# Optimization experiments

Measured on AMD Instinct MI355X. Metric: run time of the kernel, lower is better.

The kernel has to match this reference:

```python
import jax, jax.numpy as jnp
import numpy as np

EPS = 1e-10
BETA = 1.0  # beta passed to VectorQuantizer in Encoder_conv


def _conv(x, w, b, stride, pad):
    # x: NCHW, w: OIHW
    y = jax.lax.conv_general_dilated(x, w, window_strides=stride, padding=pad,
                                     dimension_numbers=('NCHW', 'OIHW', 'NCHW'))
    if b is not None:
        y = y + b[None, :, None, None]
    return y


def _forward(x, w_in, b_in, w_h1, b_h1, w_h2, b_h2, w_h3, b_h3,
             r0_w1, r0_w2, r1_w1, r1_w2, emb):
    relu = jax.nn.relu
    h = relu(_conv(x, w_in, b_in, (2, 2), [(1, 1), (1, 1)]))      # [B,128,256,256]
    h = relu(_conv(h, w_h1, b_h1, (4, 4), [(2, 2), (2, 2)]))      # [B,256,64,64]
    h = relu(_conv(h, w_h2, b_h2, (4, 4), [(2, 2), (2, 2)]))      # [B,256,16,16]
    h = relu(_conv(h, w_h3, b_h3, (2, 2), [(1, 1), (1, 1)]))      # [B,256,8,8]
    # ResidualBlock with 2 Residual layers: relu->conv[1,3]->relu->conv[1,1], no bias
    for wa, wb in ((r0_w1, r0_w2), (r1_w1, r1_w2)):
        t = _conv(relu(h), wa, None, (1, 1), [(0, 0), (1, 1)])
        t = _conv(relu(t), wb, None, (1, 1), [(0, 0), (0, 0)])
        h = h + t
    h = relu(h)
    # VectorQuantizer
    lat = jnp.transpose(h, (0, 2, 3, 1))                          # [B,H,W,D]
    D = emb.shape[1]
    flat = lat.reshape(-1, D)                                     # [N,D]
    dist = (jnp.sum(flat * flat, axis=1, keepdims=True)
            + jnp.sum(emb * emb, axis=1)
            - 2.0 * flat @ emb.T)                                 # [N,K]
    idx = jnp.argmin(dist, axis=1)                                # [N]
    quant = emb[idx].reshape(lat.shape)                           # [B,H,W,D]
    sg = jax.lax.stop_gradient
    e_loss = jnp.mean((sg(quant) - lat) ** 2)
    q_loss = jnp.mean((quant - sg(lat)) ** 2)
    loss = q_loss + BETA * e_loss
    quant_st = lat + sg(quant - lat)                              # straight-through
    probs = jnp.mean(jax.nn.one_hot(idx, emb.shape[0], dtype=lat.dtype), axis=0)
    perplexity = jnp.exp(-jnp.sum(probs * jnp.log(probs + EPS)))
    return jnp.transpose(quant_st, (0, 3, 1, 2)), loss, perplexity


def setup_inputs() -> dict:
    key = jax.random.key(0)
    ks = jax.random.split(key, 14)
    C_in, C, K = 3, 256, 512
    s = 0.05
    f32 = jnp.float32
    return {
        'x':     jax.random.normal(ks[0], (8, C_in, 512, 512), f32),
        'w_in':  jax.random.normal(ks[1], (C // 2, C_in, 4, 4), f32) * s,
        'b_in':  jnp.zeros((C // 2,), f32),
        'w_h1':  jax.random.normal(ks[2], (C, C // 2, 7, 7), f32) * s,
        'b_h1':  jnp.zeros((C,), f32),
        'w_h2':  jax.random.normal(ks[3], (C, C, 7, 7), f32) * s,
        'b_h2':  jnp.zeros((C,), f32),
        'w_h3':  jax.random.normal(ks[4], (C, C, 3, 3), f32) * s,
        'b_h3':  jnp.zeros((C,), f32),
        'r0_w1': jax.random.normal(ks[5], (4 * C, C, 1, 3), f32) * s,
        'r0_w2': jax.random.normal(ks[6], (C, 4 * C, 1, 1), f32) * s,
        'r1_w1': jax.random.normal(ks[7], (4 * C, C, 1, 3), f32) * s,
        'r1_w2': jax.random.normal(ks[8], (C, 4 * C, 1, 1), f32) * s,
        'emb':   jax.random.uniform(ks[9], (K, C), f32, -1.0 / K, 1.0 / K),
    }


def reference(x, w_in, b_in, w_h1, b_h1, w_h2, b_h2, w_h3, b_h3,
              r0_w1, r0_w2, r1_w1, r1_w2, emb):
    return _forward(x, w_in, b_in, w_h1, b_h1, w_h2, b_h2, w_h3, b_h3,
                    r0_w1, r0_w2, r1_w1, r1_w2, emb)
```

## Files before the change

kernel.cpp:

```cpp
#include <hip/hip_runtime.h>
#include <hip/hip_bf16.h>

typedef __hip_bfloat16 bf16;
typedef __attribute__((ext_vector_type(4))) float f32x4;
typedef __attribute__((ext_vector_type(8))) short short8;

__device__ __forceinline__ float b2f(bf16 v) { return __bfloat162float(v); }
__device__ __forceinline__ ushort f2bu(float v)
{
    bf16 b = __float2bfloat16(v);
    return *(ushort*)&b;
}
__device__ __forceinline__ uint relu2(uint v)
{
    uint r = v;
    if (r & 0x8000u)     r &= 0xFFFF0000u;
    if (r & 0x80000000u) r &= 0x0000FFFFu;
    return r;
}
__device__ __forceinline__ uint packbf2(float a, float b)
{
    uint lo = f2bu(a), hi = f2bu(b);
    return lo | (hi << 16);
}

typedef const __attribute__((address_space(1))) unsigned int* as1_u32;
typedef __attribute__((address_space(3))) unsigned int* as3_u32;
__device__ __forceinline__ void gld16(const void* g, uint* l)
{
    __builtin_amdgcn_global_load_lds((as1_u32)g, (as3_u32)l, 16, 0, 0);
}

__global__ __launch_bounds__(256) void initw_k(
        const float* __restrict__ w_in, const float* __restrict__ w_h1,
        const float* __restrict__ w_h2, const float* __restrict__ w_h3,
        const float* __restrict__ r0w1, const float* __restrict__ r0w2,
        const float* __restrict__ r1w1, const float* __restrict__ r1w2,
        const float* __restrict__ emb,
        bf16* __restrict__ wp1, bf16* __restrict__ wpack2, bf16* __restrict__ wpack3,
        bf16* __restrict__ wp4, bf16* __restrict__ wpA0, bf16* __restrict__ wpA1,
        bf16* __restrict__ wpB0, bf16* __restrict__ wpB1,
        float* __restrict__ en, float* __restrict__ mse, int* __restrict__ hist,
        float* __restrict__ zpad)
{
    __shared__ ushort ls[12544];
    int b = blockIdx.x, t = threadIdx.x;

    if (b < 256) {
        const float* src = w_h1 + (size_t)b * 6272;
        for (int i = t; i < 6272; i += 256) ls[i] = f2bu(src[i]);
        __syncthreads();
        for (int e = t; e < 800; e += 256) {
            int tap = e >> 4, cib8 = e & 15;
            short8 v;
            #pragma unroll
            for (int cil = 0; cil < 8; ++cil)
                v[cil] = (tap < 49) ? (short)ls[(cib8 * 8 + cil) * 49 + tap] : (short)0;
            *(short8*)(wpack2 + ((size_t)(tap * 16 + cib8) * 256 + b) * 8) = v;
        }
        return;
    }
    if (b < 512) {
        int co = b - 256;
        const float* src = w_h2 + (size_t)co * 12544;
        for (int i = t; i < 12544; i += 256) ls[i] = f2bu(src[i]);
        __syncthreads();
        for (int e = t; e < 1600; e += 256) {
            int tap = e >> 5, cib8 = e & 31;
            short8 v;
            #pragma unroll
            for (int cil = 0; cil < 8; ++cil)
                v[cil] = (tap < 49) ? (short)ls[(cib8 * 8 + cil) * 49 + tap] : (short)0;
            *(short8*)(wpack3 + ((size_t)(tap * 32 + cib8) * 256 + co) * 8) = v;
        }
        return;
    }
    if (b < 768) {
        int co = b - 512;
        const float* src = w_h3 + (size_t)co * 2304;
        for (int i = t; i < 2304; i += 256) ls[i] = f2bu(src[i]);
        __syncthreads();
        for (int e = t; e < 288; e += 256) {
            int tap = e >> 5, cib8 = e & 31;
            short8 v;
            #pragma unroll
            for (int cil = 0; cil < 8; ++cil)
                v[cil] = (short)ls[(cib8 * 8 + cil) * 9 + tap];
            *(short8*)(wp4 + ((size_t)(tap * 32 + cib8) * 256 + co) * 8) = v;
        }
        return;
    }
    if (b < 2816) {
        int r = b - 768;
        int which = r >> 10;
        int co = r & 1023;
        const float* srcb = which ? r1w1 : r0w1;
        bf16* dstb = which ? wpA1 : wpA0;
        const float* src = srcb + (size_t)co * 768;
        for (int i = t; i < 768; i += 256) ls[i] = f2bu(src[i]);
        __syncthreads();
        if (t < 96) {
            int tap = t >> 5, cib8 = t & 31;
            short8 v;
            #pragma unroll
            for (int cil = 0; cil < 8; ++cil)
                v[cil] = (short)ls[(cib8 * 8 + cil) * 3 + tap];
            *(short8*)(dstb + ((size_t)(tap * 32 + cib8) * 1024 + co) * 8) = v;
        }
        return;
    }
    if (b < 3072) {
        int r = b - 2816;
        int which = r >> 7;
        const float* srcb = which ? r1w2 : r0w2;
        bf16* dstb = which ? wpB1 : wpB0;
        int c = (r & 127) * 256 + t;
        int cib8 = c >> 8, co = c & 255;
        const float* s = srcb + (size_t)co * 1024 + cib8 * 8;
        short8 v;
        #pragma unroll
        for (int cil = 0; cil < 8; ++cil) v[cil] = (short)f2bu(s[cil]);
        *(short8*)(dstb + (size_t)c * 8) = v;
        return;
    }
    if (b < 3104) {
        int i = (b - 3072) * 256 + t;
        int j = i & 7; int co = (i >> 3) & 127; int kb = i >> 10;
        int k = kb * 8 + j;
        wp1[i] = __float2bfloat16(k < 48 ? w_in[co * 48 + k] : 0.f);
        return;
    }
    if (b < 3106) {
        int row = (b - 3104) * 256 + t;
        const float4* e = (const float4*)(emb + (size_t)row * 256);
        float s = 0.f;
        for (int d4 = 0; d4 < 64; ++d4) {
            float4 v = e[d4];
            s += v.x * v.x + v.y * v.y + v.z * v.z + v.w * v.w;
        }
        en[row] = s;
        return;
    }
    if (t == 0) mse[0] = 0.f;
    for (int i = t; i < 512; i += 256) hist[i] = 0;
    if (t < 64) zpad[t] = 0.f;
}

__global__ __launch_bounds__(256) void conv1m_k(const float* __restrict__ x,
        const bf16* __restrict__ wp1, const float* __restrict__ bias,
        bf16* __restrict__ h1c)
{
    int bid = blockIdx.x;
    int pxt = bid & 511, img = bid >> 9;
    int tr = pxt >> 4, tc = pxt & 15;
    int oh0 = tr * 8, ow0 = tc * 16;
    const float* xi = x + (size_t)img * 786432;
    bf16* oT = h1c + (size_t)img * 8388608;

    int t = threadIdx.x;
    int wave = t >> 6, lane = t & 63;
    int quad = lane >> 4, l15 = lane & 15;

    __shared__ ushort xs[4 * 640];
    __shared__ ushort ot[128 * 136];

    int ihb = oh0 * 2 - 1, iwb = ow0 * 2 - 1;
    for (int i = t; i < 1836; i += 256) {
        int ci = i / 612; int r1 = i - ci * 612;
        int ihl = r1 / 34, iwl = r1 - ihl * 34;
        int ih = ihb + ihl, iw = iwb + iwl;
        float v = 0.f;
        if ((unsigned)ih < 512u && (unsigned)iw < 512u)
            v = xi[ci * 262144 + ih * 512 + iw];
        xs[ci * 640 + ihl * 35 + iwl] = f2bu(v);
    }
    for (int i = t; i < 640; i += 256) xs[3 * 640 + i] = 0;
    __syncthreads();

    f32x4 zero = {0.f, 0.f, 0.f, 0.f};
    f32x4 acc[8][2];
    #pragma unroll
    for (int m = 0; m < 8; ++m) { acc[m][0] = zero; acc[m][1] = zero; }

    int ci_b = quad >> 1;
    int kh0 = (quad & 1) * 2;
    int iwl0 = 2 * l15;

    #pragma unroll
    for (int ks = 0; ks < 2; ++ks) {
        union { short8 v; uint u[4]; } b[2];
        #pragma unroll
        for (int nt = 0; nt < 2; ++nt) {
            int py = wave * 2 + nt;
            int base = (ks * 2 + ci_b) * 640 + (2 * py + kh0) * 35 + iwl0;
            b[nt].u[0] = *(const uint*)&xs[base];
            b[nt].u[1] = *(const uint*)&xs[base + 2];
            b[nt].u[2] = *(const uint*)&xs[base + 35];
            b[nt].u[3] = *(const uint*)&xs[base + 37];
        }
        const bf16* abase = wp1 + ((size_t)(ks * 4 + quad) * 128 + l15) * 8;
        #pragma unroll
        for (int m = 0; m < 8; ++m) {
            short8 a = *(const short8*)(abase + m * 16 * 8);
            acc[m][0] = __builtin_amdgcn_mfma_f32_16x16x32_bf16(a, b[0].v, acc[m][0], 0, 0, 0);
            acc[m][1] = __builtin_amdgcn_mfma_f32_16x16x32_bf16(a, b[1].v, acc[m][1], 0, 0, 0);
        }
    }

    #pragma unroll
    for (int m = 0; m < 8; ++m) {
        int cobase = m * 16 + quad * 4;
        float b0 = bias[cobase], b1 = bias[cobase + 1];
        float b2 = bias[cobase + 2], b3 = bias[cobase + 3];
        #pragma unroll
        for (int nt = 0; nt < 2; ++nt) {
            int pxl = (wave * 2 + nt) * 16 + l15;
            uint w0 = packbf2(fmaxf(b0 + acc[m][nt][0], 0.f),
                              fmaxf(b1 + acc[m][nt][1], 0.f));
            uint w1 = packbf2(fmaxf(b2 + acc[m][nt][2], 0.f),
                              fmaxf(b3 + acc[m][nt][3], 0.f));
            *(uint*)&ot[pxl * 136 + cobase]     = w0;
            *(uint*)&ot[pxl * 136 + cobase + 2] = w1;
        }
    }
    __syncthreads();
    {
        int pxl = t >> 1, half = t & 1;
        int oh = oh0 + (pxl >> 4), ow = ow0 + (pxl & 15);
        size_t px = (size_t)(oh * 256 + ow);
        #pragma unroll
        for (int cb = 0; cb < 4; ++cb) {
            int c16 = half * 4 + cb;
            const uint4* src = (const uint4*)&ot[pxl * 136 + c16 * 16];
            uint4* dst = (uint4*)(oT + ((size_t)c16 * 65536 + px) * 16);
            dst[0] = src[0];
            dst[1] = src[1];
        }
    }
}

template <int IH, int OH, int CI, int SPLIT, int MODE>
__global__ __launch_bounds__(256, 2) void conv_mfma9_k(
        const bf16* __restrict__ inC, const bf16* __restrict__ wpack,
        const float* __restrict__ bias, float* __restrict__ outA,
        bf16* __restrict__ outT, const float* __restrict__ zpad)
{
    constexpr int TPD = OH / 8;
    constexpr int NT = TPD * TPD;
    constexpr int CPB = (CI / 16) / SPLIT;
    constexpr int CIB8 = CI / 8;
    constexpr int NPX = IH * IH;
    constexpr int SLOTS = 2496;

    int bid = blockIdx.x;
    int pxt = bid % NT;
    int rest = bid / NT;
    int img = rest & 7;
    int split = rest >> 3;
    int oh0 = (pxt / TPD) * 8, ow0 = (pxt % TPD) * 8;

    int t = threadIdx.x;
    int wave = t >> 6, lane = t & 63;
    int quad = lane >> 4, l15 = lane & 15;

    const bf16* inb = inC + (size_t)img * ((size_t)NPX * CI);

    __shared__ __align__(16) uint bufA[SLOTS * 4];
    __shared__ __align__(16) uint bufB[SLOTS * 4];

    f32x4 zero = {0.f, 0.f, 0.f, 0.f};
    f32x4 acc[4][4];
    #pragma unroll
    for (int a = 0; a < 4; ++a)
        #pragma unroll
        for (int b = 0; b < 4; ++b) acc[a][b] = zero;

    int ihb = oh0 * 4 - 2, iwb = ow0 * 4 - 2;
    int qxl = l15 & 7, pyl = l15 >> 3;
    int tap_par = quad >> 1, ci_half = quad & 1;

    int  srel[10];
    bool sval[10];
    #pragma unroll
    for (int it = 0; it < 10; ++it) {
        int sb = (it < 9) ? it * 256 + wave * 64 : 2304 + wave * 64;
        int p  = sb + lane;
        int pb = p << 4;
        int lb = pb ^ (((pb >> 7) & 7) << 4);
        int j  = lb >> 4;
        int pos = j >> 1, half = j & 1;
        int r = pos / 35, c = pos - r * 35;
        int ih = ihb + r, iw = iwb + c;
        sval[it] = (j < 2450) && ((unsigned)ih < (unsigned)IH)
                   && ((unsigned)iw < (unsigned)IH);
        srel[it] = (ih * IH + iw) * 16 + half * 8;
    }

    auto stage = [&](int ch, uint* dst) {
        const bf16* cbp = inb + (size_t)ch * NPX * 16;
        #pragma unroll
        for (int it = 0; it < 10; ++it) {
            if (it == 9 && wave >= 3) continue;
            int sb = (it < 9) ? it * 256 + wave * 64 : 2304 + wave * 64;
            const void* src = sval[it] ? (const void*)(cbp + srel[it])
                                       : (const void*)zpad;
            gld16(src, dst + sb * 4);
        }
    };

    int rbase = pyl * 4480 + qxl * 128 + ci_half * 16;
    int d1  = tap_par * 32;
    int d29 = tap_par * 928;

    auto compute = [&](int ch, const uint* cbuf) {
        const bf16* ab = wpack
            + ((size_t)(ch * 2 + ci_half) * 256 + wave * 64 + l15) * 8
            + (size_t)tap_par * (CIB8 * 2048);
        __builtin_amdgcn_s_setprio(1);
        short8 aC[4], bC[4], aN[4], bN[4];
        {
            #pragma unroll
            for (int ct = 0; ct < 4; ++ct)
                aC[ct] = *(const short8*)(ab + ct * 128);
            int lbb = rbase + d1;
            #pragma unroll
            for (int pt = 0; pt < 4; ++pt) {
                int lb = lbb + pt * 8960;
                int pb = lb ^ (((lb >> 7) & 7) << 4);
                bC[pt] = *(const short8*)((const char*)cbuf + pb);
            }
        }
        #pragma unroll
        for (int tp = 0; tp < 25; ++tp) {
            if (tp < 24) {
                const int tn  = tp + 1;
                const int kh0 = (2 * tn) / 7, kw0 = (2 * tn) % 7;
                const int cE  = (kh0 * 35 + kw0) * 32;
                int dsel = (tn == 24) ? 0 : ((kw0 == 6) ? d29 : d1);
                int lbb  = rbase + cE + dsel;
                const bf16* at = ab + (size_t)(2 * tn) * (CIB8 * 2048);
                #pragma unroll
                for (int ct = 0; ct < 4; ++ct)
                    aN[ct] = *(const short8*)(at + ct * 128);
                #pragma unroll
                for (int pt = 0; pt < 4; ++pt) {
                    int lb = lbb + pt * 8960;
                    int pb = lb ^ (((lb >> 7) & 7) << 4);
                    bN[pt] = *(const short8*)((const char*)cbuf + pb);
                }
            }
            #pragma unroll
            for (int pt = 0; pt < 4; ++pt)
                #pragma unroll
                for (int ct = 0; ct < 4; ++ct)
                    acc[ct][pt] = __builtin_amdgcn_mfma_f32_16x16x32_bf16(
                        aC[ct], bC[pt], acc[ct][pt], 0, 0, 0);
            if (tp < 24) {
                #pragma unroll
                for (int i = 0; i < 4; ++i) { aC[i] = aN[i]; bC[i] = bN[i]; }
            }
        }
        __builtin_amdgcn_s_setprio(0);
    };

    if constexpr (CPB == 1) {
        stage(split, bufA);
        __syncthreads();
        compute(split, bufA);
    } else {
        stage(split * CPB, bufA);
        __syncthreads();
        for (int cc2 = 0; cc2 < CPB; cc2 += 2) {
            stage(split * CPB + cc2 + 1, bufB);
            compute(split * CPB + cc2, bufA);
            __syncthreads();
            if (cc2 + 2 < CPB) stage(split * CPB + cc2 + 2, bufA);
            compute(split * CPB + cc2 + 1, bufB);
            __syncthreads();
        }
    }

    #pragma unroll
    for (int ct = 0; ct < 4; ++ct) {
        int cobase = wave * 64 + ct * 16 + quad * 4;
        #pragma unroll
        for (int pt = 0; pt < 4; ++pt) {
            int px = pt * 16 + l15;
            int oh = oh0 + (px >> 3), ow = ow0 + (px & 7);
            int pxg = oh * OH + ow;
            #pragma unroll
            for (int r = 0; r < 4; ++r) {
                int co = cobase + r;
                float v = acc[ct][pt][r];
                if (MODE == 3) {
                    outA[(size_t)split * ((size_t)8 * OH * OH * 256)
                         + (size_t)img * (OH * OH * 256)
                         + (size_t)co * (OH * OH) + pxg] = v;
                } else {
                    float o = fmaxf(bias[co] + v, 0.f);
                    size_t base = (size_t)img * (size_t)(OH * OH * 256);
                    outT[base + ((size_t)(co >> 4) * (OH * OH) + pxg) * 16 + (co & 15)]
                        = __float2bfloat16(o);
                }
            }
        }
    }
}

__global__ void combine3_k(const float* __restrict__ p3, const float* __restrict__ bias,
                           bf16* __restrict__ h3T)
{
    int idx = blockIdx.x * 256 + threadIdx.x;
    int px = idx & 255;
    int co = (idx >> 8) & 255;
    int img = idx >> 16;
    float v = bias[co];
    #pragma unroll
    for (int s = 0; s < 16; ++s) v += p3[(size_t)s * 524288 + idx];
    v = fmaxf(v, 0.f);
    h3T[((size_t)img * 256 + px) * 256 + co] = __float2bfloat16(v);
}

__global__ __launch_bounds__(256) void conv4m_k(const bf16* __restrict__ h3T,
        const bf16* __restrict__ wp4, const float* __restrict__ bias,
        bf16* __restrict__ h4T)
{
    int bid = blockIdx.x;
    int img = bid >> 2, cog = bid & 3;
    int t = threadIdx.x;
    int wave = t >> 6, lane = t & 63;
    int quad = lane >> 4, l15 = lane & 15;

    __shared__ uint pt[16 * 325];

    for (int i = t; i < 16 * 325; i += 256) pt[i] = 0;

    f32x4 zero = {0.f, 0.f, 0.f, 0.f};
    f32x4 acc[4];
    #pragma unroll
    for (int b = 0; b < 4; ++b) acc[b] = zero;

    const bf16* inb = h3T + (size_t)img * 65536;

    for (int ch = 0; ch < 8; ++ch) {
        __syncthreads();
        for (int e = t; e < 4096; e += 256) {
            int cp = e & 15, px = e >> 4;
            int py = px >> 4, qx = px & 15;
            uint v = *(const uint*)(inb + (size_t)px * 256 + ch * 32 + cp * 2);
            pt[cp * 325 + (py + 1) * 18 + qx + 1] = v;
        }
        __syncthreads();

        for (int tap = 0; tap < 9; ++tap) {
            int kh = tap / 3, kw = tap - kh * 3;
            const bf16* abase = wp4 + ((size_t)((tap * 32 + ch * 4 + quad) * 256)
                                       + cog * 64 + wave * 16 + l15) * 8;
            short8 a = *(const short8*)abase;
            #pragma unroll
            for (int pq = 0; pq < 4; ++pq) {
                int pyo = 2 * pq + (l15 >> 3);
                int ipos = (2 * pyo + kh) * 18 + 2 * (l15 & 7) + kw;
                union { short8 v; uint u[4]; } b;
                b.u[0] = pt[(quad * 4 + 0) * 325 + ipos];
                b.u[1] = pt[(quad * 4 + 1) * 325 + ipos];
                b.u[2] = pt[(quad * 4 + 2) * 325 + ipos];
                b.u[3] = pt[(quad * 4 + 3) * 325 + ipos];
                acc[pq] = __builtin_amdgcn_mfma_f32_16x16x32_bf16(
                    a, b.v, acc[pq], 0, 0, 0);
            }
        }
    }

    int cobase = cog * 64 + wave * 16 + quad * 4;
    #pragma unroll
    for (int pq = 0; pq < 4; ++pq) {
        int px = pq * 16 + l15;
        #pragma unroll
        for (int r = 0; r < 4; ++r) {
            int co = cobase + r;
            float v = fmaxf(bias[co] + acc[pq][r], 0.f);
            h4T[((size_t)img * 64 + px) * 256 + co] = __float2bfloat16(v);
        }
    }
}

__global__ __launch_bounds__(256) void resam_k(const bf16* __restrict__ hT,
        const bf16* __restrict__ wpA, bf16* __restrict__ t1T)
{
    int bid = blockIdx.x;
    int img = bid >> 3, g = bid & 7;
    int t = threadIdx.x;
    int wave = t >> 6, lane = t & 63;
    int quad = lane >> 4, l15 = lane & 15;

    __shared__ uint ph[128 * 81];

    for (int i = t; i < 128 * 81; i += 256) ph[i] = 0;
    __syncthreads();
    const bf16* inb = hT + (size_t)img * 16384;
    for (int e = t; e < 8192; e += 256) {
        int cp = e & 127, px = e >> 7;
        uint v = relu2(*(const uint*)(inb + (size_t)px * 256 + cp * 2));
        ph[cp * 81 + (px >> 3) * 10 + (px & 7) + 1] = v;
    }
    __syncthreads();

    f32x4 zero = {0.f, 0.f, 0.f, 0.f};
    f32x4 acc[2][4];
    #pragma unroll
    for (int a = 0; a < 2; ++a)
        #pragma unroll
        for (int b = 0; b < 4; ++b) acc[a][b] = zero;

    for (int ch = 0; ch < 8; ++ch) {
        for (int tap = 0; tap < 3; ++tap) {
            const bf16* abase = wpA + ((size_t)(tap * 32 + ch * 4 + quad) * 1024
                                       + g * 128 + wave * 32 + l15) * 8;
            short8 a[2];
            #pragma unroll
            for (int ct = 0; ct < 2; ++ct)
                a[ct] = *(const short8*)(abase + ct * 16 * 8);
            #pragma unroll
            for (int pq = 0; pq < 4; ++pq) {
                int py = 2 * pq + (l15 >> 3);
                int pos = py * 10 + (l15 & 7) + tap;
                union { short8 v; uint u[4]; } b;
                b.u[0] = ph[(ch * 16 + quad * 4 + 0) * 81 + pos];
                b.u[1] = ph[(ch * 16 + quad * 4 + 1) * 81 + pos];
                b.u[2] = ph[(ch * 16 + quad * 4 + 2) * 81 + pos];
                b.u[3] = ph[(ch * 16 + quad * 4 + 3) * 81 + pos];
                #pragma unroll
                for (int ct = 0; ct < 2; ++ct)
                    acc[ct][pq] = __builtin_amdgcn_mfma_f32_16x16x32_bf16(
                        a[ct], b.v, acc[ct][pq], 0, 0, 0);
            }
        }
    }

    #pragma unroll
    for (int ct = 0; ct < 2; ++ct) {
        int cobase = g * 128 + wave * 32 + ct * 16 + quad * 4;
        #pragma unroll
        for (int pq = 0; pq < 4; ++pq) {
            int px = pq * 16 + l15;
            #pragma unroll
            for (int r = 0; r < 4; ++r)
                t1T[((size_t)img * 64 + px) * 1024 + cobase + r]
                    = __float2bfloat16(acc[ct][pq][r]);
        }
    }
}

__global__ __launch_bounds__(256) void resbm_k(const bf16* __restrict__ holdT,
        const bf16* __restrict__ t1T, const bf16* __restrict__ wpB,
        bf16* __restrict__ hnewT)
{
    int bid = blockIdx.x;
    int img = bid >> 2, cog = bid & 3;
    int t = threadIdx.x;
    int wave = t >> 6, lane = t & 63;
    int quad = lane >> 4, l15 = lane & 15;

    __shared__ uint pb[256 * 65];

    f32x4 zero = {0.f, 0.f, 0.f, 0.f};
    f32x4 acc[4];
    #pragma unroll
    for (int b = 0; b < 4; ++b) acc[b] = zero;

    const bf16* inb = t1T + (size_t)img * 65536;

    for (int s = 0; s < 2; ++s) {
        __syncthreads();
        for (int e = t; e < 16384; e += 256) {
            int cp = e & 255, px = e >> 8;
            uint v = relu2(*(const uint*)(inb + (size_t)px * 1024 + s * 512 + cp * 2));
            pb[cp * 65 + px] = v;
        }
        __syncthreads();

        for (int chl = 0; chl < 16; ++chl) {
            int ch = s * 16 + chl;
            const bf16* abase = wpB + ((size_t)(ch * 4 + quad) * 256
                                       + cog * 64 + wave * 16 + l15) * 8;
            short8 a = *(const short8*)abase;
            #pragma unroll
            for (int pq = 0; pq < 4; ++pq) {
                int px = pq * 16 + l15;
                union { short8 v; uint u[4]; } b;
                b.u[0] = pb[(chl * 16 + quad * 4 + 0) * 65 + px];
                b.u[1] = pb[(chl * 16 + quad * 4 + 1) * 65 + px];
                b.u[2] = pb[(chl * 16 + quad * 4 + 2) * 65 + px];
                b.u[3] = pb[(chl * 16 + quad * 4 + 3) * 65 + px];
                acc[pq] = __builtin_amdgcn_mfma_f32_16x16x32_bf16(
                    a, b.v, acc[pq], 0, 0, 0);
            }
        }
    }

    int cobase = cog * 64 + wave * 16 + quad * 4;
    #pragma unroll
    for (int pq = 0; pq < 4; ++pq) {
        int px = pq * 16 + l15;
        #pragma unroll
        for (int r = 0; r < 4; ++r) {
            int co = cobase + r;
            size_t o = ((size_t)img * 64 + px) * 256 + co;
            float v = b2f(holdT[o]) + acc[pq][r];
            hnewT[o] = __float2bfloat16(v);
        }
    }
}

__global__ __launch_bounds__(256) void vq_k(const bf16* __restrict__ h6T,
        const float* __restrict__ emb, const float* __restrict__ en,
        float* __restrict__ out, float* __restrict__ mse_acc, int* __restrict__ hist)
{
    int row0 = blockIdx.x * 4;
    int t = threadIdx.x;
    int wave = t >> 6, lane = t & 63;
    __shared__ float lat[4][256];
    __shared__ float swd[4][4];
    __shared__ int   swi[4][4];
    __shared__ int   fidx[4];
    __shared__ float smse[4];

    for (int e = t; e < 1024; e += 256) {
        int r = e >> 8, c = e & 255;
        lat[r][c] = fmaxf(b2f(h6T[(size_t)(row0 + r) * 256 + c]), 0.f);
    }
    __syncthreads();

    float a0[4] = {0.f, 0.f, 0.f, 0.f}, a1[4] = {0.f, 0.f, 0.f, 0.f};
    const float4* e0 = (const float4*)(emb + (size_t)t * 256);
    const float4* e1 = (const float4*)(emb + (size_t)(t + 256) * 256);
    for (int d4 = 0; d4 < 64; ++d4) {
        float4 v0 = e0[d4], v1 = e1[d4];
        #pragma unroll
        for (int r = 0; r < 4; ++r) {
            float l0 = lat[r][d4 * 4], l1 = lat[r][d4 * 4 + 1];
            float l2 = lat[r][d4 * 4 + 2], l3 = lat[r][d4 * 4 + 3];
            a0[r] += l0 * v0.x + l1 * v0.y + l2 * v0.z + l3 * v0.w;
            a1[r] += l0 * v1.x + l1 * v1.y + l2 * v1.z + l3 * v1.w;
        }
    }
    float en0 = en[t], en1 = en[t + 256];
    float bd[4]; int bi[4];
    #pragma unroll
    for (int r = 0; r < 4; ++r) {
        float d0 = en0 - 2.f * a0[r], d1v = en1 - 2.f * a1[r];
        bd[r] = d0; bi[r] = t;
        if (d1v < bd[r]) { bd[r] = d1v; bi[r] = t + 256; }
    }
    #pragma unroll
    for (int s = 1; s < 64; s <<= 1) {
        #pragma unroll
        for (int r = 0; r < 4; ++r) {
            float od = __shfl_xor(bd[r], s);
            int   oi = __shfl_xor(bi[r], s);
            if (od < bd[r] || (od == bd[r] && oi < bi[r])) { bd[r] = od; bi[r] = oi; }
        }
    }
    if (lane == 0) {
        #pragma unroll
        for (int r = 0; r < 4; ++r) { swd[wave][r] = bd[r]; swi[wave][r] = bi[r]; }
    }
    __syncthreads();
    if (t < 4) {
        float best = swd[0][t]; int bidx = swi[0][t];
        for (int w = 1; w < 4; ++w) {
            float od = swd[w][t]; int oi = swi[w][t];
            if (od < best || (od == best && oi < bidx)) { best = od; bidx = oi; }
        }
        fidx[t] = bidx;
    }
    __syncthreads();

    float msel = 0.f;
    #pragma unroll
    for (int r = 0; r < 4; ++r) {
        int row = row0 + r;
        int b = row >> 6, y = (row >> 3) & 7, xx = row & 7;
        float q = emb[(size_t)fidx[r] * 256 + t];
        out[((size_t)(b * 256 + t) * 8 + y) * 8 + xx] = q;
        float diff = q - lat[r][t];
        msel += diff * diff;
    }
    #pragma unroll
    for (int s = 1; s < 64; s <<= 1) msel += __shfl_xor(msel, s);
    if (lane == 0) smse[wave] = msel;
    __syncthreads();
    if (t == 0) atomicAdd(mse_acc, smse[0] + smse[1] + smse[2] + smse[3]);
    if (t < 4) atomicAdd(&hist[fidx[t]], 1);
}

__global__ void final_k(const float* __restrict__ mse_acc, const int* __restrict__ hist,
                        float* __restrict__ out)
{
    __shared__ float sh[512];
    int t = threadIdx.x;
    float p = (float)hist[t] / 512.f;
    sh[t] = p * logf(p + 1e-10f);
    __syncthreads();
    for (int s = 256; s > 0; s >>= 1) {
        if (t < s) sh[t] += sh[t + s];
        __syncthreads();
    }
    if (t == 0) {
        float loss = 2.f * mse_acc[0] / (512.f * 256.f);
        float perp = expf(-sh[0]);
        out[131072] = loss;
        out[131073] = perp;
    }
}

extern "C" void kernel_launch(void* const* d_in, const int* in_sizes, int n_in,
                              void* d_out, int out_size, void* d_ws, size_t ws_size,
                              hipStream_t stream)
{
    const float* x    = (const float*)d_in[0];
    const float* w_in = (const float*)d_in[1];
    const float* b_in = (const float*)d_in[2];
    const float* w_h1 = (const float*)d_in[3];
    const float* b_h1 = (const float*)d_in[4];
    const float* w_h2 = (const float*)d_in[5];
    const float* b_h2 = (const float*)d_in[6];
    const float* w_h3 = (const float*)d_in[7];
    const float* b_h3 = (const float*)d_in[8];
    const float* r0w1 = (const float*)d_in[9];
    const float* r0w2 = (const float*)d_in[10];
    const float* r1w1 = (const float*)d_in[11];
    const float* r1w2 = (const float*)d_in[12];
    const float* emb  = (const float*)d_in[13];
    float* out = (float*)d_out;

    char* ws = (char*)d_ws;
    size_t off = 0;
    auto alloc = [&](size_t bytes) -> void* {
        void* p = ws + off;
        off += (bytes + 255) & ~(size_t)255;
        return p;
    };

    float* en  = (float*)alloc(512 * 4);
    float* mse = (float*)alloc(256);
    int*  hist = (int*)alloc(512 * 4);
    float* zpad = (float*)alloc(256);
    float* p3  = (float*)alloc(8388608ull * 4);
    bf16* h3T  = (bf16*)alloc(524288ull * 2);
    bf16* h4T  = (bf16*)alloc(131072ull * 2);
    bf16* t1T  = (bf16*)alloc(524288ull * 2);
    bf16* h5T  = (bf16*)alloc(131072ull * 2);
    bf16* h6T  = (bf16*)alloc(131072ull * 2);
    bf16* wp1  = (bf16*)alloc(8192ull * 2);
    bf16* wpack2 = (bf16*)alloc(1638400ull * 2);
    bf16* wpack3 = (bf16*)alloc(3276800ull * 2);
    bf16* wp4  = (bf16*)alloc(589824ull * 2);
    bf16* wpA0 = (bf16*)alloc(786432ull * 2);
    bf16* wpA1 = (bf16*)alloc(786432ull * 2);
    bf16* wpB0 = (bf16*)alloc(262144ull * 2);
    bf16* wpB1 = (bf16*)alloc(262144ull * 2);
    bf16* h2c  = (bf16*)alloc(8388608ull * 2);
    size_t base_end = off;

    const size_t H1F_B = 8388608ull * 8 * 2;
    size_t needT1 = base_end + H1F_B + 4096;
    bf16* h1c;
    int tier;
    if (ws_size >= needT1) {
        h1c = (bf16*)alloc(H1F_B);
        tier = 1;
    } else {
        h1c = (bf16*)alloc(8388608ull * 2);
        tier = 2;
    }

    initw_k<<<3107, 256, 0, stream>>>(w_in, w_h1, w_h2, w_h3, r0w1, r0w2, r1w1, r1w2,
        emb, wp1, wpack2, wpack3, wp4, wpA0, wpA1, wpB0, wpB1, en, mse, hist, zpad);

    if (tier == 1) {
        conv1m_k<<<4096, 256, 0, stream>>>(x, wp1, b_in, h1c);
        conv_mfma9_k<256, 64, 128, 1, 0><<<512, 256, 0, stream>>>(
            h1c, wpack2, b_h1, nullptr, h2c, zpad);
    } else {
        for (int n = 0; n < 8; ++n) {
            conv1m_k<<<512, 256, 0, stream>>>(x + (size_t)n * 786432, wp1, b_in, h1c);
            conv_mfma9_k<256, 64, 128, 1, 0><<<64, 256, 0, stream>>>(
                h1c, wpack2, b_h1, nullptr, h2c + (size_t)n * 1048576, zpad);
        }
    }

    conv_mfma9_k<64, 16, 256, 16, 3><<<512, 256, 0, stream>>>(
        h2c, wpack3, nullptr, p3, nullptr, zpad);
    combine3_k<<<2048, 256, 0, stream>>>(p3, b_h2, h3T);

    conv4m_k<<<32, 256, 0, stream>>>(h3T, wp4, b_h3, h4T);
    resam_k<<<64, 256, 0, stream>>>(h4T, wpA0, t1T);
    resbm_k<<<32, 256, 0, stream>>>(h4T, t1T, wpB0, h5T);
    resam_k<<<64, 256, 0, stream>>>(h5T, wpA1, t1T);
    resbm_k<<<32, 256, 0, stream>>>(h5T, t1T, wpB1, h6T);

    vq_k<<<128, 256, 0, stream>>>(h6T, emb, en, out, mse, hist);
    final_k<<<1, 512, 0, stream>>>(mse, hist, out);
}
```

Baseline: 464.4 us.

## Vectorize conv epilogue stores, halve conv3 split-K, and widen small-kernel grids

Conv epilogue writes for the non-split mode now pack four bf16 outputs into one 8-byte store instead of four scalar stores. The conv3 split-K factor drops from 16 to 8, which halves the partial buffer and the combine reads but gives fewer blocks. The residual kernels and the VQ kernel are split into twice as many blocks with less work each, to fill more CUs on the tiny tail layers. This trades less per-block reuse and more redundant staging for more parallelism.

After: 444.3 us (median of 2 runs). -4.3%, faster.

```diff
diff --git a/kernel.cpp b/kernel.cpp
--- a/kernel.cpp
+++ b/kernel.cpp
@@ -388,20 +388,26 @@
             int px = pt * 16 + l15;
             int oh = oh0 + (px >> 3), ow = ow0 + (px & 7);
             int pxg = oh * OH + ow;
-            #pragma unroll
-            for (int r = 0; r < 4; ++r) {
-                int co = cobase + r;
-                float v = acc[ct][pt][r];
-                if (MODE == 3) {
+            if (MODE == 3) {
+                #pragma unroll
+                for (int r = 0; r < 4; ++r) {
+                    int co = cobase + r;
                     outA[(size_t)split * ((size_t)8 * OH * OH * 256)
                          + (size_t)img * (OH * OH * 256)
-                         + (size_t)co * (OH * OH) + pxg] = v;
-                } else {
-                    float o = fmaxf(bias[co] + v, 0.f);
-                    size_t base = (size_t)img * (size_t)(OH * OH * 256);
-                    outT[base + ((size_t)(co >> 4) * (OH * OH) + pxg) * 16 + (co & 15)]
-                        = __float2bfloat16(o);
+                         + (size_t)co * (OH * OH) + pxg] = acc[ct][pt][r];
                 }
+            } else {
+                float o0 = fmaxf(bias[cobase]     + acc[ct][pt][0], 0.f);
+                float o1 = fmaxf(bias[cobase + 1] + acc[ct][pt][1], 0.f);
+                float o2 = fmaxf(bias[cobase + 2] + acc[ct][pt][2], 0.f);
+                float o3 = fmaxf(bias[cobase + 3] + acc[ct][pt][3], 0.f);
+                uint2 w;
+                w.x = packbf2(o0, o1);
+                w.y = packbf2(o2, o3);
+                size_t base = (size_t)img * (size_t)(OH * OH * 256);
+                *(uint2*)(outT + base
+                          + ((size_t)(wave * 4 + ct) * (OH * OH) + pxg) * 16
+                          + quad * 4) = w;
             }
         }
     }
@@ -416,7 +422,7 @@
     int img = idx >> 16;
     float v = bias[co];
     #pragma unroll
-    for (int s = 0; s < 16; ++s) v += p3[(size_t)s * 524288 + idx];
+    for (int s = 0; s < 8; ++s) v += p3[(size_t)s * 524288 + idx];
     v = fmaxf(v, 0.f);
     h3T[((size_t)img * 256 + px) * 256 + co] = __float2bfloat16(v);
 }
@@ -489,7 +495,7 @@
         const bf16* __restrict__ wpA, bf16* __restrict__ t1T)
 {
     int bid = blockIdx.x;
-    int img = bid >> 3, g = bid & 7;
+    int img = bid >> 4, g = bid & 15;
     int t = threadIdx.x;
     int wave = t >> 6, lane = t & 63;
     int quad = lane >> 4, l15 = lane & 15;
@@ -507,20 +513,15 @@
     __syncthreads();
 
     f32x4 zero = {0.f, 0.f, 0.f, 0.f};
-    f32x4 acc[2][4];
-    #pragma unroll
-    for (int a = 0; a < 2; ++a)
-        #pragma unroll
-        for (int b = 0; b < 4; ++b) acc[a][b] = zero;
+    f32x4 acc[4];
+    #pragma unroll
+    for (int b = 0; b < 4; ++b) acc[b] = zero;
 
     for (int ch = 0; ch < 8; ++ch) {
         for (int tap = 0; tap < 3; ++tap) {
             const bf16* abase = wpA + ((size_t)(tap * 32 + ch * 4 + quad) * 1024
-                                       + g * 128 + wave * 32 + l15) * 8;
-            short8 a[2];
-            #pragma unroll
-            for (int ct = 0; ct < 2; ++ct)
-                a[ct] = *(const short8*)(abase + ct * 16 * 8);
+                                       + g * 64 + wave * 16 + l15) * 8;
+            short8 a = *(const short8*)abase;
             #pragma unroll
             for (int pq = 0; pq < 4; ++pq) {
                 int py = 2 * pq + (l15 >> 3);
@@ -530,25 +531,20 @@
                 b.u[1] = ph[(ch * 16 + quad * 4 + 1) * 81 + pos];
                 b.u[2] = ph[(ch * 16 + quad * 4 + 2) * 81 + pos];
                 b.u[3] = ph[(ch * 16 + quad * 4 + 3) * 81 + pos];
-                #pragma unroll
-                for (int ct = 0; ct < 2; ++ct)
-                    acc[ct][pq] = __builtin_amdgcn_mfma_f32_16x16x32_bf16(
-                        a[ct], b.v, acc[ct][pq], 0, 0, 0);
+                acc[pq] = __builtin_amdgcn_mfma_f32_16x16x32_bf16(
+                    a, b.v, acc[pq], 0, 0, 0);
             }
         }
     }
 
-    #pragma unroll
-    for (int ct = 0; ct < 2; ++ct) {
-        int cobase = g * 128 + wave * 32 + ct * 16 + quad * 4;
-        #pragma unroll
-        for (int pq = 0; pq < 4; ++pq) {
-            int px = pq * 16 + l15;
-            #pragma unroll
-            for (int r = 0; r < 4; ++r)
-                t1T[((size_t)img * 64 + px) * 1024 + cobase + r]
-                    = __float2bfloat16(acc[ct][pq][r]);
-        }
+    int cobase = g * 64 + wave * 16 + quad * 4;
+    #pragma unroll
+    for (int pq = 0; pq < 4; ++pq) {
+        int px = pq * 16 + l15;
+        #pragma unroll
+        for (int r = 0; r < 4; ++r)
+            t1T[((size_t)img * 64 + px) * 1024 + cobase + r]
+                = __float2bfloat16(acc[pq][r]);
     }
 }
 
@@ -557,26 +553,25 @@
         bf16* __restrict__ hnewT)
 {
     int bid = blockIdx.x;
-    int img = bid >> 2, cog = bid & 3;
+    int img = bid >> 3, cog = (bid >> 1) & 3, ph = bid & 1;
     int t = threadIdx.x;
     int wave = t >> 6, lane = t & 63;
     int quad = lane >> 4, l15 = lane & 15;
 
-    __shared__ uint pb[256 * 65];
+    __shared__ uint pb[256 * 33];
 
     f32x4 zero = {0.f, 0.f, 0.f, 0.f};
-    f32x4 acc[4];
-    #pragma unroll
-    for (int b = 0; b < 4; ++b) acc[b] = zero;
-
-    const bf16* inb = t1T + (size_t)img * 65536;
+    f32x4 acc[2];
+    acc[0] = zero; acc[1] = zero;
+
+    const bf16* inb = t1T + (size_t)img * 65536 + (size_t)ph * 32 * 1024;
 
     for (int s = 0; s < 2; ++s) {
         __syncthreads();
-        for (int e = t; e < 16384; e += 256) {
-            int cp = e & 255, px = e >> 8;
-            uint v = relu2(*(const uint*)(inb + (size_t)px * 1024 + s * 512 + cp * 2));
-            pb[cp * 65 + px] = v;
+        for (int e = t; e < 8192; e += 256) {
+            int cp = e & 255, pxl = e >> 8;
+            uint v = relu2(*(const uint*)(inb + (size_t)pxl * 1024 + s * 512 + cp * 2));
+            pb[cp * 33 + pxl] = v;
         }
         __syncthreads();
 
@@ -586,13 +581,13 @@
                                        + cog * 64 + wave * 16 + l15) * 8;
             short8 a = *(const short8*)abase;
             #pragma unroll
-            for (int pq = 0; pq < 4; ++pq) {
-                int px = pq * 16 + l15;
+            for (int pq = 0; pq < 2; ++pq) {
+                int pxl = pq * 16 + l15;
                 union { short8 v; uint u[4]; } b;
-                b.u[0] = pb[(chl * 16 + quad * 4 + 0) * 65 + px];
-                b.u[1] = pb[(chl * 16 + quad * 4 + 1) * 65 + px];
-                b.u[2] = pb[(chl * 16 + quad * 4 + 2) * 65 + px];
-                b.u[3] = pb[(chl * 16 + quad * 4 + 3) * 65 + px];
+                b.u[0] = pb[(chl * 16 + quad * 4 + 0) * 33 + pxl];
+                b.u[1] = pb[(chl * 16 + quad * 4 + 1) * 33 + pxl];
+                b.u[2] = pb[(chl * 16 + quad * 4 + 2) * 33 + pxl];
+                b.u[3] = pb[(chl * 16 + quad * 4 + 3) * 33 + pxl];
                 acc[pq] = __builtin_amdgcn_mfma_f32_16x16x32_bf16(
                     a, b.v, acc[pq], 0, 0, 0);
             }
@@ -601,8 +596,8 @@
 
     int cobase = cog * 64 + wave * 16 + quad * 4;
     #pragma unroll
-    for (int pq = 0; pq < 4; ++pq) {
-        int px = pq * 16 + l15;
+    for (int pq = 0; pq < 2; ++pq) {
+        int px = ph * 32 + pq * 16 + l15;
         #pragma unroll
         for (int r = 0; r < 4; ++r) {
             int co = cobase + r;
@@ -617,28 +612,28 @@
         const float* __restrict__ emb, const float* __restrict__ en,
         float* __restrict__ out, float* __restrict__ mse_acc, int* __restrict__ hist)
 {
-    int row0 = blockIdx.x * 4;
+    int row0 = blockIdx.x * 2;
     int t = threadIdx.x;
     int wave = t >> 6, lane = t & 63;
-    __shared__ float lat[4][256];
-    __shared__ float swd[4][4];
-    __shared__ int   swi[4][4];
-    __shared__ int   fidx[4];
+    __shared__ float lat[2][256];
+    __shared__ float swd[4][2];
+    __shared__ int   swi[4][2];
+    __shared__ int   fidx[2];
     __shared__ float smse[4];
 
-    for (int e = t; e < 1024; e += 256) {
+    for (int e = t; e < 512; e += 256) {
         int r = e >> 8, c = e & 255;
         lat[r][c] = fmaxf(b2f(h6T[(size_t)(row0 + r) * 256 + c]), 0.f);
     }
     __syncthreads();
 
-    float a0[4] = {0.f, 0.f, 0.f, 0.f}, a1[4] = {0.f, 0.f, 0.f, 0.f};
+    float a0[2] = {0.f, 0.f}, a1[2] = {0.f, 0.f};
     const float4* e0 = (const float4*)(emb + (size_t)t * 256);
     const float4* e1 = (const float4*)(emb + (size_t)(t + 256) * 256);
     for (int d4 = 0; d4 < 64; ++d4) {
         float4 v0 = e0[d4], v1 = e1[d4];
         #pragma unroll
-        for (int r = 0; r < 4; ++r) {
+        for (int r = 0; r < 2; ++r) {
             float l0 = lat[r][d4 * 4], l1 = lat[r][d4 * 4 + 1];
             float l2 = lat[r][d4 * 4 + 2], l3 = lat[r][d4 * 4 + 3];
             a0[r] += l0 * v0.x + l1 * v0.y + l2 * v0.z + l3 * v0.w;
@@ -646,9 +641,9 @@
         }
     }
     float en0 = en[t], en1 = en[t + 256];
-    float bd[4]; int bi[4];
-    #pragma unroll
-    for (int r = 0; r < 4; ++r) {
+    float bd[2]; int bi[2];
+    #pragma unroll
+    for (int r = 0; r < 2; ++r) {
         float d0 = en0 - 2.f * a0[r], d1v = en1 - 2.f * a1[r];
         bd[r] = d0; bi[r] = t;
         if (d1v < bd[r]) { bd[r] = d1v; bi[r] = t + 256; }
@@ -656,7 +651,7 @@
     #pragma unroll
     for (int s = 1; s < 64; s <<= 1) {
         #pragma unroll
-        for (int r = 0; r < 4; ++r) {
+        for (int r = 0; r < 2; ++r) {
             float od = __shfl_xor(bd[r], s);
             int   oi = __shfl_xor(bi[r], s);
             if (od < bd[r] || (od == bd[r] && oi < bi[r])) { bd[r] = od; bi[r] = oi; }
@@ -664,10 +659,10 @@
     }
     if (lane == 0) {
         #pragma unroll
-        for (int r = 0; r < 4; ++r) { swd[wave][r] = bd[r]; swi[wave][r] = bi[r]; }
+        for (int r = 0; r < 2; ++r) { swd[wave][r] = bd[r]; swi[wave][r] = bi[r]; }
     }
     __syncthreads();
-    if (t < 4) {
+    if (t < 2) {
         float best = swd[0][t]; int bidx = swi[0][t];
         for (int w = 1; w < 4; ++w) {
             float od = swd[w][t]; int oi = swi[w][t];
@@ -679,7 +674,7 @@
 
     float msel = 0.f;
     #pragma unroll
-    for (int r = 0; r < 4; ++r) {
+    for (int r = 0; r < 2; ++r) {
         int row = row0 + r;
         int b = row >> 6, y = (row >> 3) & 7, xx = row & 7;
         float q = emb[(size_t)fidx[r] * 256 + t];
@@ -692,7 +687,7 @@
     if (lane == 0) smse[wave] = msel;
     __syncthreads();
     if (t == 0) atomicAdd(mse_acc, smse[0] + smse[1] + smse[2] + smse[3]);
-    if (t < 4) atomicAdd(&hist[fidx[t]], 1);
+    if (t < 2) atomicAdd(&hist[fidx[t]], 1);
 }
 
 __global__ void final_k(const float* __restrict__ mse_acc, const int* __restrict__ hist,
@@ -747,7 +742,7 @@
     float* mse = (float*)alloc(256);
     int*  hist = (int*)alloc(512 * 4);
     float* zpad = (float*)alloc(256);
-    float* p3  = (float*)alloc(8388608ull * 4);
+    float* p3  = (float*)alloc(4194304ull * 4);
     bf16* h3T  = (bf16*)alloc(524288ull * 2);
     bf16* h4T  = (bf16*)alloc(131072ull * 2);
     bf16* t1T  = (bf16*)alloc(524288ull * 2);
@@ -791,16 +786,16 @@
         }
     }
 
-    conv_mfma9_k<64, 16, 256, 16, 3><<<512, 256, 0, stream>>>(
+    conv_mfma9_k<64, 16, 256, 8, 3><<<256, 256, 0, stream>>>(
         h2c, wpack3, nullptr, p3, nullptr, zpad);
     combine3_k<<<2048, 256, 0, stream>>>(p3, b_h2, h3T);
 
     conv4m_k<<<32, 256, 0, stream>>>(h3T, wp4, b_h3, h4T);
-    resam_k<<<64, 256, 0, stream>>>(h4T, wpA0, t1T);
-    resbm_k<<<32, 256, 0, stream>>>(h4T, t1T, wpB0, h5T);
-    resam_k<<<64, 256, 0, stream>>>(h5T, wpA1, t1T);
-    resbm_k<<<32, 256, 0, stream>>>(h5T, t1T, wpB1, h6T);
-
-    vq_k<<<128, 256, 0, stream>>>(h6T, emb, en, out, mse, hist);
+    resam_k<<<128, 256, 0, stream>>>(h4T, wpA0, t1T);
+    resbm_k<<<64, 256, 0, stream>>>(h4T, t1T, wpB0, h5T);
+    resam_k<<<128, 256, 0, stream>>>(h5T, wpA1, t1T);
+    resbm_k<<<64, 256, 0, stream>>>(h5T, t1T, wpB1, h6T);
+
+    vq_k<<<256, 256, 0, stream>>>(h6T, emb, en, out, mse, hist);
     final_k<<<1, 512, 0, stream>>>(mse, hist, out);
 }
```
